# Kernel optimization log

Hardware: AMD Instinct MI355X
Metric: run time of the kernel (lower is better)

The kernel has to match this reference:

```python
import jax, jax.numpy as jnp
import numpy as np

IN_CH, IN_DIM, OUT_CH, OUT_DIM = 16, 32, 32, 32
NUM_ITERS = 3
EPS = 1e-11


def setup_inputs() -> dict:
    key = jax.random.key(0)
    kx, kw = jax.random.split(key)
    B, N = 32, 128
    x = jax.random.normal(kx, (B, N, IN_CH, IN_DIM), dtype=jnp.float32)
    # learned transform, matches torch Parameter randn(1,1,in_ch,out_ch,in_dim,out_dim)
    W = jax.random.normal(kw, (IN_CH, OUT_CH, IN_DIM, OUT_DIM), dtype=jnp.float32)
    return {"x": x, "W": W, "number_of_nodes": N}


def squash(s):
    # s: [B, 1, out_ch, out_dim]; squash along capsule dim (axis=3)
    mag_sq = jnp.sum(s * s, axis=3, keepdims=True)
    mag = jnp.sqrt(mag_sq) + EPS
    a_j = mag_sq / (1.0 + mag_sq)
    return a_j * (s / mag), a_j


def reference(x, W, number_of_nodes):
    B, N = x.shape[0], x.shape[1]
    # u_hat[b,n,c,o,j] = sum_i x[b,n,c,i] * W[c,o,i,j]
    u_hat = jnp.einsum('bnci,coij->bncoj', x, W)
    u_hat = u_hat.reshape(B, N * IN_CH, OUT_CH, OUT_DIM)

    b_ij = jnp.zeros((B, N * IN_CH, OUT_CH, 1), dtype=u_hat.dtype)
    v_j = a_j = None
    for _ in range(NUM_ITERS):
        c_ij = jax.nn.softmax(b_ij, axis=1)          # softmax over input capsules
        s_j = jnp.sum(c_ij * u_hat, axis=1, keepdims=True)  # [B,1,out_ch,out_dim]
        v_j, a_j = squash(s_j)
        # agreement: broadcast v_j over input-capsule dim (no explicit cat)
        u_vj = jnp.sum(u_hat * v_j, axis=3, keepdims=True)
        b_ij = b_ij + u_vj
    return v_j, a_j
```

## Files before the change

### kernel.cpp

```cpp
#include <hip/hip_runtime.h>
#include <math.h>

#define BB 32
#define NN 128
#define CC 16
#define OO 32
#define II 32
#define JJ 32
#define MM (NN*CC)
static constexpr float EPS_ = 1e-11f;


__global__ __launch_bounds__(1024) void k_transpose(
    const float* __restrict__ x, float* __restrict__ xT,
    float* __restrict__ x4T) {
  int b = blockIdx.x >> 4, c = blockIdx.x & 15;
  __shared__ __align__(16) float xsT[II][NN + 4];
  int tid = threadIdx.x;
  {
    int n = tid >> 3, i4 = (tid & 7) * 4;
    float4 v = *(const float4*)(x + (((size_t)(b * NN + n)) * CC + c) * II + i4);
    xsT[i4 + 0][n] = v.x; xsT[i4 + 1][n] = v.y;
    xsT[i4 + 2][n] = v.z; xsT[i4 + 3][n] = v.w;
  }
  __syncthreads();
  {
    int i = tid >> 5, n4 = tid & 31;
    float4 v = *(const float4*)(&xsT[i][n4 * 4]);
    ((float4*)(xT + ((size_t)(b * CC + c)) * II * NN))[tid] = v;
  }
  {
    int nf4 = tid >> 5, i = tid & 31;
    float4 v = make_float4(xsT[i][nf4 * 4 + 0], xsT[i][nf4 * 4 + 1],
                           xsT[i][nf4 * 4 + 2], xsT[i][nf4 * 4 + 3]);
    ((float4*)(x4T + ((size_t)(b * CC + c)) * II * NN))[tid] = v;
  }
}

__global__ __launch_bounds__(1024, 4) void k_route(
    const float* __restrict__ xT, const float* __restrict__ x4T,
    const float* __restrict__ W, float* __restrict__ out) {
  int bid = blockIdx.x;
  int b = bid & 31, o0 = (bid >> 5) * 2;
  int tid = threadIdx.x;

  __shared__ __align__(16) float bijL[2][CC][NN];
  __shared__ __align__(16) float coef[2][CC][NN];
  __shared__ float cxs[2][CC][II];
  __shared__ float wv [2][CC][II];
  __shared__ float partA[2][CC][JJ];
  __shared__ float vs[2][JJ];
  __shared__ float redM[CC][2], redE[CC][2];

  {
    int o = tid >> 9, c = (tid >> 5) & 15, n4 = tid & 31;
    *(float4*)(&bijL[o][c][n4 * 4]) = make_float4(0.f, 0.f, 0.f, 0.f);
    float u = 1.0f / (float)MM;
    *(float4*)(&coef[o][c][n4 * 4]) = make_float4(u, u, u, u);
  }

  float wA[II];
  {
    int o = tid >> 9, c = (tid >> 5) & 15, j = tid & 31;
    const float* Wp = W + (((size_t)(c * OO + o0 + o)) * II) * JJ + j;
    #pragma unroll
    for (int i = 0; i < II; ++i) wA[i] = Wp[i * JJ];
  }
  float4 wW[8];
  {
    int o = tid >> 9, c = (tid >> 5) & 15, i = tid & 31;
    const float4* Wr = (const float4*)(W + (((size_t)(c * OO + o0 + o)) * II + i) * JJ);
    #pragma unroll
    for (int q = 0; q < 8; ++q) wW[q] = Wr[q];
  }

  const float4* xTb  = (const float4*)(xT  + (size_t)b * CC * II * NN);
  const float4* x4Tb = (const float4*)(x4T + (size_t)b * CC * II * NN);
  __syncthreads();

  for (int it = 0; it < 3; ++it) {
    {
      int c = tid >> 6, l = tid & 63, i = l & 31, nh = l >> 5;
      const float4* xr = x4Tb + c * (II * NN / 4) + l;
      float a0 = 0.f, a1 = 0.f;
      #pragma unroll 4
      for (int q = 0; q < 16; ++q) {
        float4 xv = xr[q * 64];
        int nf = 2 * q + nh;
        float4 f0 = *(const float4*)(&coef[0][c][nf * 4]);
        float4 f1 = *(const float4*)(&coef[1][c][nf * 4]);
        a0 += xv.x * f0.x + xv.y * f0.y + xv.z * f0.z + xv.w * f0.w;
        a1 += xv.x * f1.x + xv.y * f1.y + xv.z * f1.z + xv.w * f1.w;
      }
      a0 += __shfl_xor(a0, 32);
      a1 += __shfl_xor(a1, 32);
      if (nh == 0) cxs[0][c][i] = a0;
      else         cxs[1][c][i] = a1;
    }
    __syncthreads();

    {
      int o = tid >> 9, c = (tid >> 5) & 15, j = tid & 31;
      float acc = 0.f;
      #pragma unroll
      for (int i = 0; i < II; ++i)
        acc += cxs[o][c][i] * wA[i];
      partA[o][c][j] = acc;
    }
    __syncthreads();

    if (tid < 64) {
      int o = tid >> 5, j = tid & 31;
      float s = 0.f;
      #pragma unroll
      for (int c = 0; c < CC; ++c) s += partA[o][c][j];
      float msq = s * s;
      #pragma unroll
      for (int off = 16; off > 0; off >>= 1) msq += __shfl_xor(msq, off);
      float mag = sqrtf(msq) + EPS_;
      float a   = msq / (1.0f + msq);
      float vv  = a * s / mag;
      if (it == 2) {
        int row = b * OO + (o0 + o);
        out[(size_t)row * JJ + j] = vv;
        if (j == 0) out[BB * OO * JJ + row] = a;
      } else {
        vs[o][j] = vv;
      }
    }
    if (it == 2) break;
    __syncthreads();

    {
      int o = tid >> 9, c = (tid >> 5) & 15, i = tid & 31;
      float acc = 0.f;
      #pragma unroll
      for (int q = 0; q < 8; ++q) {
        acc += wW[q].x * vs[o][q*4+0] + wW[q].y * vs[o][q*4+1]
             + wW[q].z * vs[o][q*4+2] + wW[q].w * vs[o][q*4+3];
      }
      wv[o][c][i] = acc;
    }
    __syncthreads();

    {
      int c = tid >> 6, n4 = (tid >> 1) & 31, s = tid & 1;
      float4 ac0 = make_float4(0.f,0.f,0.f,0.f);
      float4 ac1 = make_float4(0.f,0.f,0.f,0.f);
      #pragma unroll 4
      for (int q = 0; q < 16; ++q) {
        int i = s * 16 + q;
        float4 xv = xTb[c * (II * NN / 4) + i * (NN / 4) + n4];
        float w0 = wv[0][c][i], w1 = wv[1][c][i];
        ac0.x += xv.x * w0; ac0.y += xv.y * w0; ac0.z += xv.z * w0; ac0.w += xv.w * w0;
        ac1.x += xv.x * w1; ac1.y += xv.y * w1; ac1.z += xv.z * w1; ac1.w += xv.w * w1;
      }
      ac0.x += __shfl_xor(ac0.x, 1); ac0.y += __shfl_xor(ac0.y, 1);
      ac0.z += __shfl_xor(ac0.z, 1); ac0.w += __shfl_xor(ac0.w, 1);
      ac1.x += __shfl_xor(ac1.x, 1); ac1.y += __shfl_xor(ac1.y, 1);
      ac1.z += __shfl_xor(ac1.z, 1); ac1.w += __shfl_xor(ac1.w, 1);
      float4 r = (s == 0) ? ac0 : ac1;
      float4 bb = *(const float4*)(&bijL[s][c][n4 * 4]);
      r.x += bb.x; r.y += bb.y; r.z += bb.z; r.w += bb.w;
      *(float4*)(&bijL[s][c][n4 * 4]) = r;

      float m4 = fmaxf(fmaxf(r.x, r.y), fmaxf(r.z, r.w));
      #pragma unroll
      for (int off = 2; off <= 32; off <<= 1) m4 = fmaxf(m4, __shfl_xor(m4, off));
      int wave = tid >> 6;
      if ((tid & 63) <= 1) redM[wave][s] = m4;
      __syncthreads();
      float mo = redM[0][s];
      #pragma unroll
      for (int w2 = 1; w2 < CC; ++w2) mo = fmaxf(mo, redM[w2][s]);
      float ex = __expf(r.x - mo), ey = __expf(r.y - mo),
            ez = __expf(r.z - mo), ew = __expf(r.w - mo);
      float e = ex + ey + ez + ew;
      #pragma unroll
      for (int off = 2; off <= 32; off <<= 1) e += __shfl_xor(e, off);
      if ((tid & 63) <= 1) redE[wave][s] = e;
      __syncthreads();
      float ss = redE[0][s];
      #pragma unroll
      for (int w2 = 1; w2 < CC; ++w2) ss += redE[w2][s];
      float rin = 1.0f / ss;
      *(float4*)(&coef[s][c][n4 * 4]) =
          make_float4(ex * rin, ey * rin, ez * rin, ew * rin);
    }
    __syncthreads();
  }
}

extern "C" void kernel_launch(void* const* d_in, const int* in_sizes, int n_in,
                              void* d_out, int out_size, void* d_ws, size_t ws_size,
                              hipStream_t stream) {
  const float* x = (const float*)d_in[0];
  const float* W = (const float*)d_in[1];
  (void)in_sizes; (void)n_in;
  float* out = (float*)d_out; (void)out_size;

  float* xT  = (float*)d_ws;
  float* x4T = xT + (size_t)BB * CC * II * NN;
  (void)ws_size;

  k_transpose<<<BB * CC, 1024, 0, stream>>>(x, xT, x4T);
  k_route<<<BB * (OO / 2), 1024, 0, stream>>>(xT, x4T, W, out);
}
```

Before: 122.9 us.

## Keep x tile in registers across routing iterations, drop second transposed copy

Each thread now loads its 16 float4 slice of the transposed x once into registers and reuses it for both the weighted-sum and agreement phases in every iteration. The cx reduction becomes a butterfly shuffle transpose-reduce, which removes the need for the second transposed buffer x4T and its writes in the transpose kernel. W is no longer held in registers; it is re-read from global memory inside each iteration. This is meant to cut repeated global reads of x and one full workspace write, in exchange for more global W traffic and more shuffles.

```diff
diff --git a/kernel.cpp b/kernel.cpp
--- a/kernel.cpp
+++ b/kernel.cpp
@@ -12,8 +12,7 @@
 
 
 __global__ __launch_bounds__(1024) void k_transpose(
-    const float* __restrict__ x, float* __restrict__ xT,
-    float* __restrict__ x4T) {
+    const float* __restrict__ x, float* __restrict__ xT) {
   int b = blockIdx.x >> 4, c = blockIdx.x & 15;
   __shared__ __align__(16) float xsT[II][NN + 4];
   int tid = threadIdx.x;
@@ -29,17 +28,11 @@
     float4 v = *(const float4*)(&xsT[i][n4 * 4]);
     ((float4*)(xT + ((size_t)(b * CC + c)) * II * NN))[tid] = v;
   }
-  {
-    int nf4 = tid >> 5, i = tid & 31;
-    float4 v = make_float4(xsT[i][nf4 * 4 + 0], xsT[i][nf4 * 4 + 1],
-                           xsT[i][nf4 * 4 + 2], xsT[i][nf4 * 4 + 3]);
-    ((float4*)(x4T + ((size_t)(b * CC + c)) * II * NN))[tid] = v;
-  }
 }
 
 __global__ __launch_bounds__(1024, 4) void k_route(
-    const float* __restrict__ xT, const float* __restrict__ x4T,
-    const float* __restrict__ W, float* __restrict__ out) {
+    const float* __restrict__ xT, const float* __restrict__ W,
+    float* __restrict__ out) {
   int bid = blockIdx.x;
   int b = bid & 31, o0 = (bid >> 5) * 2;
   int tid = threadIdx.x;
@@ -52,108 +45,128 @@
   __shared__ float vs[2][JJ];
   __shared__ float redM[CC][2], redE[CC][2];
 
+  int l = tid & 63;
+  int c = tid >> 6, n4 = l >> 1, s = l & 1;
+  const float4* xTb = (const float4*)(xT + (size_t)b * CC * II * NN);
+  const float4* xp  = xTb + c * (II * NN / 4) + (s * 16) * (NN / 4) + n4;
+  float4 xv[16];
+  #pragma unroll
+  for (int q = 0; q < 16; ++q) xv[q] = xp[q * (NN / 4)];
+
   {
-    int o = tid >> 9, c = (tid >> 5) & 15, n4 = tid & 31;
-    *(float4*)(&bijL[o][c][n4 * 4]) = make_float4(0.f, 0.f, 0.f, 0.f);
+    int o = tid >> 9, ci = (tid >> 5) & 15, m4i = tid & 31;
+    *(float4*)(&bijL[o][ci][m4i * 4]) = make_float4(0.f, 0.f, 0.f, 0.f);
     float u = 1.0f / (float)MM;
-    *(float4*)(&coef[o][c][n4 * 4]) = make_float4(u, u, u, u);
-  }
-
-  float wA[II];
-  {
-    int o = tid >> 9, c = (tid >> 5) & 15, j = tid & 31;
-    const float* Wp = W + (((size_t)(c * OO + o0 + o)) * II) * JJ + j;
-    #pragma unroll
-    for (int i = 0; i < II; ++i) wA[i] = Wp[i * JJ];
-  }
-  float4 wW[8];
-  {
-    int o = tid >> 9, c = (tid >> 5) & 15, i = tid & 31;
-    const float4* Wr = (const float4*)(W + (((size_t)(c * OO + o0 + o)) * II + i) * JJ);
-    #pragma unroll
-    for (int q = 0; q < 8; ++q) wW[q] = Wr[q];
-  }
-
-  const float4* xTb  = (const float4*)(xT  + (size_t)b * CC * II * NN);
-  const float4* x4Tb = (const float4*)(x4T + (size_t)b * CC * II * NN);
+    *(float4*)(&coef[o][ci][m4i * 4]) = make_float4(u, u, u, u);
+  }
   __syncthreads();
 
   for (int it = 0; it < 3; ++it) {
     {
-      int c = tid >> 6, l = tid & 63, i = l & 31, nh = l >> 5;
-      const float4* xr = x4Tb + c * (II * NN / 4) + l;
-      float a0 = 0.f, a1 = 0.f;
-      #pragma unroll 4
+      float4 cf0 = *(const float4*)(&coef[0][c][n4 * 4]);
+      float4 cf1 = *(const float4*)(&coef[1][c][n4 * 4]);
+      float p0[16], p1[16];
+      #pragma unroll
       for (int q = 0; q < 16; ++q) {
-        float4 xv = xr[q * 64];
-        int nf = 2 * q + nh;
-        float4 f0 = *(const float4*)(&coef[0][c][nf * 4]);
-        float4 f1 = *(const float4*)(&coef[1][c][nf * 4]);
-        a0 += xv.x * f0.x + xv.y * f0.y + xv.z * f0.z + xv.w * f0.w;
-        a1 += xv.x * f1.x + xv.y * f1.y + xv.z * f1.z + xv.w * f1.w;
-      }
-      a0 += __shfl_xor(a0, 32);
-      a1 += __shfl_xor(a1, 32);
-      if (nh == 0) cxs[0][c][i] = a0;
-      else         cxs[1][c][i] = a1;
-    }
-    __syncthreads();
-
-    {
-      int o = tid >> 9, c = (tid >> 5) & 15, j = tid & 31;
+        p0[q] = xv[q].x*cf0.x + xv[q].y*cf0.y + xv[q].z*cf0.z + xv[q].w*cf0.w;
+        p1[q] = xv[q].x*cf1.x + xv[q].y*cf1.y + xv[q].z*cf1.z + xv[q].w*cf1.w;
+      }
+      bool u2 = (l >> 1) & 1, u4 = (l >> 2) & 1, u8 = (l >> 3) & 1, u16 = (l >> 4) & 1;
+      #pragma unroll
+      for (int k = 0; k < 8; ++k) {
+        float s0 = u2 ? p0[k] : p0[k+8], s1 = u2 ? p1[k] : p1[k+8];
+        float r0 = __shfl_xor(s0, 2),   r1 = __shfl_xor(s1, 2);
+        p0[k] = (u2 ? p0[k+8] : p0[k]) + r0;
+        p1[k] = (u2 ? p1[k+8] : p1[k]) + r1;
+      }
+      #pragma unroll
+      for (int k = 0; k < 4; ++k) {
+        float s0 = u4 ? p0[k] : p0[k+4], s1 = u4 ? p1[k] : p1[k+4];
+        float r0 = __shfl_xor(s0, 4),   r1 = __shfl_xor(s1, 4);
+        p0[k] = (u4 ? p0[k+4] : p0[k]) + r0;
+        p1[k] = (u4 ? p1[k+4] : p1[k]) + r1;
+      }
+      #pragma unroll
+      for (int k = 0; k < 2; ++k) {
+        float s0 = u8 ? p0[k] : p0[k+2], s1 = u8 ? p1[k] : p1[k+2];
+        float r0 = __shfl_xor(s0, 8),   r1 = __shfl_xor(s1, 8);
+        p0[k] = (u8 ? p0[k+2] : p0[k]) + r0;
+        p1[k] = (u8 ? p1[k+2] : p1[k]) + r1;
+      }
+      {
+        float s0 = u16 ? p0[0] : p0[1], s1 = u16 ? p1[0] : p1[1];
+        float r0 = __shfl_xor(s0, 16),  r1 = __shfl_xor(s1, 16);
+        p0[0] = (u16 ? p0[1] : p0[0]) + r0;
+        p1[0] = (u16 ? p1[1] : p1[0]) + r1;
+      }
+      p0[0] += __shfl_xor(p0[0], 32);
+      p1[0] += __shfl_xor(p1[0], 32);
+      if ((l & 32) == 0) {
+        int qf = (u2 ? 8 : 0) + (u4 ? 4 : 0) + (u8 ? 2 : 0) + (u16 ? 1 : 0);
+        cxs[0][c][s * 16 + qf] = p0[0];
+        cxs[1][c][s * 16 + qf] = p1[0];
+      }
+    }
+    __syncthreads();
+
+    {
+      int o = tid >> 9, cA = (tid >> 5) & 15, j = tid & 31;
+      const float* Wp = W + (((size_t)(cA * OO + o0 + o)) * II) * JJ + j;
       float acc = 0.f;
-      #pragma unroll
+      #pragma unroll 8
       for (int i = 0; i < II; ++i)
-        acc += cxs[o][c][i] * wA[i];
-      partA[o][c][j] = acc;
+        acc += cxs[o][cA][i] * Wp[i * JJ];
+      partA[o][cA][j] = acc;
     }
     __syncthreads();
 
     if (tid < 64) {
       int o = tid >> 5, j = tid & 31;
-      float s = 0.f;
-      #pragma unroll
-      for (int c = 0; c < CC; ++c) s += partA[o][c][j];
-      float msq = s * s;
+      float sA = 0.f;
+      #pragma unroll
+      for (int cR = 0; cR < CC; ++cR) sA += partA[o][cR][j];
+      float msq = sA * sA;
       #pragma unroll
       for (int off = 16; off > 0; off >>= 1) msq += __shfl_xor(msq, off);
       float mag = sqrtf(msq) + EPS_;
       float a   = msq / (1.0f + msq);
-      float vv  = a * s / mag;
+      float vvq = a * sA / mag;
       if (it == 2) {
         int row = b * OO + (o0 + o);
-        out[(size_t)row * JJ + j] = vv;
+        out[(size_t)row * JJ + j] = vvq;
         if (j == 0) out[BB * OO * JJ + row] = a;
       } else {
-        vs[o][j] = vv;
+        vs[o][j] = vvq;
       }
     }
     if (it == 2) break;
     __syncthreads();
 
     {
-      int o = tid >> 9, c = (tid >> 5) & 15, i = tid & 31;
+      int o = tid >> 9, cW = (tid >> 5) & 15, i = tid & 31;
+      const float4* Wr = (const float4*)(W + (((size_t)(cW * OO + o0 + o)) * II + i) * JJ);
       float acc = 0.f;
-      #pragma unroll
+      #pragma unroll 4
       for (int q = 0; q < 8; ++q) {
-        acc += wW[q].x * vs[o][q*4+0] + wW[q].y * vs[o][q*4+1]
-             + wW[q].z * vs[o][q*4+2] + wW[q].w * vs[o][q*4+3];
-      }
-      wv[o][c][i] = acc;
-    }
-    __syncthreads();
-
-    {
-      int c = tid >> 6, n4 = (tid >> 1) & 31, s = tid & 1;
+        float4 w4 = Wr[q];
+        acc += w4.x * vs[o][q*4+0] + w4.y * vs[o][q*4+1]
+             + w4.z * vs[o][q*4+2] + w4.w * vs[o][q*4+3];
+      }
+      wv[o][cW][i] = acc;
+    }
+    __syncthreads();
+
+    {
       float4 ac0 = make_float4(0.f,0.f,0.f,0.f);
       float4 ac1 = make_float4(0.f,0.f,0.f,0.f);
-      #pragma unroll 4
+      #pragma unroll
       for (int q = 0; q < 16; ++q) {
         int i = s * 16 + q;
-        float4 xv = xTb[c * (II * NN / 4) + i * (NN / 4) + n4];
         float w0 = wv[0][c][i], w1 = wv[1][c][i];
-        ac0.x += xv.x * w0; ac0.y += xv.y * w0; ac0.z += xv.z * w0; ac0.w += xv.w * w0;
-        ac1.x += xv.x * w1; ac1.y += xv.y * w1; ac1.z += xv.z * w1; ac1.w += xv.w * w1;
+        ac0.x += xv[q].x * w0; ac0.y += xv[q].y * w0;
+        ac0.z += xv[q].z * w0; ac0.w += xv[q].w * w0;
+        ac1.x += xv[q].x * w1; ac1.y += xv[q].y * w1;
+        ac1.z += xv[q].z * w1; ac1.w += xv[q].w * w1;
       }
       ac0.x += __shfl_xor(ac0.x, 1); ac0.y += __shfl_xor(ac0.y, 1);
       ac0.z += __shfl_xor(ac0.z, 1); ac0.w += __shfl_xor(ac0.w, 1);
@@ -199,10 +212,9 @@
   (void)in_sizes; (void)n_in;
   float* out = (float*)d_out; (void)out_size;
 
-  float* xT  = (float*)d_ws;
-  float* x4T = xT + (size_t)BB * CC * II * NN;
+  float* xT = (float*)d_ws;
   (void)ws_size;
 
-  k_transpose<<<BB * CC, 1024, 0, stream>>>(x, xT, x4T);
-  k_route<<<BB * (OO / 2), 1024, 0, stream>>>(xT, x4T, W, out);
+  k_transpose<<<BB * CC, 1024, 0, stream>>>(x, xT);
+  k_route<<<BB * (OO / 2), 1024, 0, stream>>>(xT, W, out);
 }
```

Result: faster. 119.2 us (-3.0%).
